# Kernel tuning notes

Measured on AMD Instinct MI355X. Metric: run time of the kernel, lower is better.

The kernel has to match this reference:

```python
import jax, jax.numpy as jnp
import numpy as np

IC = 196        # number of input channels / recurrence steps
B, N = 32, 8192 # batch, points per batch


def setup_inputs() -> dict:
    key = jax.random.key(0)
    ks = jax.random.split(key, 9)
    n = IC - 1  # 195 ReLU cells
    # stacked weights for the 195 distinct rnn cells: Linear(2,6)->ReLU->Linear(6,1)->ReLU
    W1 = jax.random.normal(ks[0], (n, 2, 6), dtype=jnp.float32) * (1.0 / np.sqrt(2.0))
    b1 = jax.random.normal(ks[1], (n, 6), dtype=jnp.float32) * 0.05
    W2 = jax.random.normal(ks[2], (n, 6, 1), dtype=jnp.float32) * (1.0 / np.sqrt(6.0))
    b2 = jax.random.normal(ks[3], (n, 1), dtype=jnp.float32) * 0.05
    # final sigmoid cell: Linear(2,6)->ReLU->Linear(6,1)->Sigmoid
    Wf1 = jax.random.normal(ks[4], (2, 6), dtype=jnp.float32) * (1.0 / np.sqrt(2.0))
    bf1 = jax.random.normal(ks[5], (6,), dtype=jnp.float32) * 0.05
    Wf2 = jax.random.normal(ks[6], (6, 1), dtype=jnp.float32) * (1.0 / np.sqrt(6.0))
    bf2 = jax.random.normal(ks[7], (1,), dtype=jnp.float32) * 0.05
    x = jax.random.normal(ks[8], (B, N, IC), dtype=jnp.float32)
    return {"x": x, "W1": W1, "b1": b1, "W2": W2, "b2": b2,
            "Wf1": Wf1, "bf1": bf1, "Wf2": Wf2, "bf2": bf2}


def reference(x, W1, b1, W2, b2, Wf1, bf1, Wf2, bf2):
    # x: [B, N, IC]. Recurrence: y0 = x[..., 0:1]; for i in 0..IC-2:
    #   y = relu_cell_i(concat(x[..., i:i+1], y));  final: sigmoid cell on x[..., IC-1].
    xs = jnp.moveaxis(x, -1, 0)          # [IC, B, N]
    y0 = xs[0][..., None]                # [B, N, 1]

    def step(y, inp):
        xi, w1, bb1, w2, bb2 = inp
        z = jnp.concatenate([xi[..., None], y], axis=-1)        # [B, N, 2]
        h = jax.nn.relu(jnp.einsum('bni,io->bno', z, w1) + bb1)  # [B, N, 6]
        y = jax.nn.relu(jnp.einsum('bnh,ho->bno', h, w2) + bb2)  # [B, N, 1]
        return y, None

    y, _ = jax.lax.scan(step, y0, (xs[:IC - 1], W1, b1, W2, b2))
    zf = jnp.concatenate([xs[IC - 1][..., None], y], axis=-1)    # [B, N, 2]
    hf = jax.nn.relu(jnp.einsum('bni,io->bno', zf, Wf1) + bf1)
    return jax.nn.sigmoid(jnp.einsum('bnh,ho->bno', hf, Wf2) + bf2)  # [B, N, 1]
```

## Files before the change

kernel.cpp:

```cpp
#include <hip/hip_runtime.h>
#include <math.h>

#define ICC 196
#define CH  16
#define NPH 12
#define RS  257
#define BLK 256

__device__ __forceinline__ float cell_step(float xi, float y, int i,
    const float* __restrict__ W1, const float* __restrict__ b1,
    const float* __restrict__ W2, const float* __restrict__ b2)
{
    const float* w1 = W1 + i * 12;
    const float* bb = b1 + i * 6;
    const float* w2 = W2 + i * 6;
    float h0 = fmaxf(fmaf(y, w1[6],  fmaf(xi, w1[0], bb[0])), 0.0f);
    float h1 = fmaxf(fmaf(y, w1[7],  fmaf(xi, w1[1], bb[1])), 0.0f);
    float h2 = fmaxf(fmaf(y, w1[8],  fmaf(xi, w1[2], bb[2])), 0.0f);
    float h3 = fmaxf(fmaf(y, w1[9],  fmaf(xi, w1[3], bb[3])), 0.0f);
    float h4 = fmaxf(fmaf(y, w1[10], fmaf(xi, w1[4], bb[4])), 0.0f);
    float h5 = fmaxf(fmaf(y, w1[11], fmaf(xi, w1[5], bb[5])), 0.0f);
    float a0 = fmaf(h0, w2[0], fmaf(h1, w2[1], b2[i]));
    float a1 = fmaf(h2, w2[2], h3 * w2[3]);
    float a2 = fmaf(h4, w2[4], h5 * w2[5]);
    return fmaxf(a0 + (a1 + a2), 0.0f);
}

__global__ __launch_bounds__(BLK, 4) void rnn_kernel(
    const float* __restrict__ x,
    const float* __restrict__ W1,
    const float* __restrict__ b1,
    const float* __restrict__ W2,
    const float* __restrict__ b2,
    const float* __restrict__ Wf1,
    const float* __restrict__ bf1,
    const float* __restrict__ Wf2,
    const float* __restrict__ bf2,
    float* __restrict__ out,
    int npoints)
{
    __shared__ float tile[CH * RS];

    const int tid = threadIdx.x;
    const int p0  = blockIdx.x * BLK;
    const int p   = p0 + tid;

    const int rl0 = tid >> 2;
    const int q4  = (tid & 3) * 4;

    float4 rA[4];

    const int pc_self = (p < npoints) ? p : (npoints - 1);
    const float4 tail = *reinterpret_cast<const float4*>(
        x + (size_t)pc_self * ICC + 192);

    #pragma unroll
    for (int k = 0; k < 4; ++k) {
        int rl = rl0 + 64 * k;
        int pc = p0 + rl; if (pc >= npoints) pc = npoints - 1;
        rA[k] = *reinterpret_cast<const float4*>(x + (size_t)pc * ICC + 0 * CH + q4);
    }
    #pragma unroll
    for (int k = 0; k < 4; ++k) {
        int rl = rl0 + 64 * k;
        tile[(q4 + 0) * RS + rl] = rA[k].x;
        tile[(q4 + 1) * RS + rl] = rA[k].y;
        tile[(q4 + 2) * RS + rl] = rA[k].z;
        tile[(q4 + 3) * RS + rl] = rA[k].w;
    }
    #pragma unroll
    for (int k = 0; k < 4; ++k) {
        int rl = rl0 + 64 * k;
        int pc = p0 + rl; if (pc >= npoints) pc = npoints - 1;
        rA[k] = *reinterpret_cast<const float4*>(x + (size_t)pc * ICC + 1 * CH + q4);
    }
    __syncthreads();

    float y = tile[0 * RS + tid];

    #pragma unroll 1
    for (int c = 0; c < NPH; ++c) {
        float xi[CH];
        #pragma unroll
        for (int j = 0; j < CH; ++j)
            xi[j] = tile[j * RS + tid];

        if (c < NPH - 1) {
            __syncthreads();
            #pragma unroll
            for (int k = 0; k < 4; ++k) {
                int rl = rl0 + 64 * k;
                tile[(q4 + 0) * RS + rl] = rA[k].x;
                tile[(q4 + 1) * RS + rl] = rA[k].y;
                tile[(q4 + 2) * RS + rl] = rA[k].z;
                tile[(q4 + 3) * RS + rl] = rA[k].w;
            }
            if (c < NPH - 2) {
                #pragma unroll
                for (int k = 0; k < 4; ++k) {
                    int rl = rl0 + 64 * k;
                    int pc = p0 + rl; if (pc >= npoints) pc = npoints - 1;
                    rA[k] = *reinterpret_cast<const float4*>(
                        x + (size_t)pc * ICC + (c + 2) * CH + q4);
                }
            }
            __syncthreads();
        }

        #pragma unroll
        for (int j = 0; j < CH; ++j)
            y = cell_step(xi[j], y, c * CH + j, W1, b1, W2, b2);
    }

    y = cell_step(tail.x, y, 192, W1, b1, W2, b2);
    y = cell_step(tail.y, y, 193, W1, b1, W2, b2);
    y = cell_step(tail.z, y, 194, W1, b1, W2, b2);

    const float xf = tail.w;
    float h0 = fmaxf(fmaf(y, Wf1[6],  fmaf(xf, Wf1[0], bf1[0])), 0.0f);
    float h1 = fmaxf(fmaf(y, Wf1[7],  fmaf(xf, Wf1[1], bf1[1])), 0.0f);
    float h2 = fmaxf(fmaf(y, Wf1[8],  fmaf(xf, Wf1[2], bf1[2])), 0.0f);
    float h3 = fmaxf(fmaf(y, Wf1[9],  fmaf(xf, Wf1[3], bf1[3])), 0.0f);
    float h4 = fmaxf(fmaf(y, Wf1[10], fmaf(xf, Wf1[4], bf1[4])), 0.0f);
    float h5 = fmaxf(fmaf(y, Wf1[11], fmaf(xf, Wf1[5], bf1[5])), 0.0f);
    float a0 = fmaf(h0, Wf2[0], fmaf(h1, Wf2[1], bf2[0]));
    float a1 = fmaf(h2, Wf2[2], h3 * Wf2[3]);
    float a2 = fmaf(h4, Wf2[4], h5 * Wf2[5]);
    float t  = a0 + (a1 + a2);

    if (p < npoints)
        out[p] = 1.0f / (1.0f + __expf(-t));
}

extern "C" void kernel_launch(void* const* d_in, const int* in_sizes, int n_in,
                              void* d_out, int out_size, void* d_ws, size_t ws_size,
                              hipStream_t stream) {
    const float* x   = (const float*)d_in[0];
    const float* W1  = (const float*)d_in[1];
    const float* b1  = (const float*)d_in[2];
    const float* W2  = (const float*)d_in[3];
    const float* b2  = (const float*)d_in[4];
    const float* Wf1 = (const float*)d_in[5];
    const float* bf1 = (const float*)d_in[6];
    const float* Wf2 = (const float*)d_in[7];
    const float* bf2 = (const float*)d_in[8];
    float* out = (float*)d_out;

    const int npoints = out_size;
    const int grid = (npoints + BLK - 1) / BLK;
    rnn_kernel<<<grid, BLK, 0, stream>>>(x, W1, b1, W2, b2,
                                         Wf1, bf1, Wf2, bf2, out, npoints);
}
```

Before: 104.6 us.

## Stage cell weights in LDS and double-buffer input chunks with explicit waitcnts

Copies all 195 cells' weights into shared memory once per block, padded to a 24-float stride, so each cell's weights come from vector LDS loads instead of scalar global loads. The input tile changes from a transposed column-major layout to a row-per-point layout read as float4. Two register buffers now alternate for the next chunk, and hand-placed s_waitcnt and s_barrier calls replace __syncthreads to overlap global loads with compute. This adds about 19KB of LDS per block, which may lower occupancy, and the inline-asm wait counts are fragile.

```diff
diff --git a/kernel.cpp b/kernel.cpp
--- a/kernel.cpp
+++ b/kernel.cpp
@@ -1,29 +1,40 @@
 #include <hip/hip_runtime.h>
 #include <math.h>
 
-#define ICC 196
-#define CH  16
-#define NPH 12
-#define RS  257
-#define BLK 256
+#define ICC   196
+#define CH    16
+#define NPH   12
+#define RS2   20
+#define BLK   256
+#define NCELL 195
+#define WSTR  24
 
-__device__ __forceinline__ float cell_step(float xi, float y, int i,
-    const float* __restrict__ W1, const float* __restrict__ b1,
-    const float* __restrict__ W2, const float* __restrict__ b2)
-{
-    const float* w1 = W1 + i * 12;
-    const float* bb = b1 + i * 6;
-    const float* w2 = W2 + i * 6;
-    float h0 = fmaxf(fmaf(y, w1[6],  fmaf(xi, w1[0], bb[0])), 0.0f);
-    float h1 = fmaxf(fmaf(y, w1[7],  fmaf(xi, w1[1], bb[1])), 0.0f);
-    float h2 = fmaxf(fmaf(y, w1[8],  fmaf(xi, w1[2], bb[2])), 0.0f);
-    float h3 = fmaxf(fmaf(y, w1[9],  fmaf(xi, w1[3], bb[3])), 0.0f);
-    float h4 = fmaxf(fmaf(y, w1[10], fmaf(xi, w1[4], bb[4])), 0.0f);
-    float h5 = fmaxf(fmaf(y, w1[11], fmaf(xi, w1[5], bb[5])), 0.0f);
-    float a0 = fmaf(h0, w2[0], fmaf(h1, w2[1], b2[i]));
-    float a1 = fmaf(h2, w2[2], h3 * w2[3]);
-    float a2 = fmaf(h4, w2[4], h5 * w2[5]);
-    return fmaxf(a0 + (a1 + a2), 0.0f);
+#define WAIT_VM(n)  asm volatile("s_waitcnt vmcnt(" #n ")" ::: "memory")
+#define WAIT_LGKM0  asm volatile("s_waitcnt lgkmcnt(0)" ::: "memory")
+#define SFENCE      __builtin_amdgcn_sched_barrier(0)
+#define SBAR        __builtin_amdgcn_s_barrier()
+
+struct WF { float4 q0,q1,q2,q3,q4,q5; float e0; };
+
+__device__ __forceinline__ WF loadWL(const float* wlds, const float* b2lds, int i) {
+    WF w;
+    const float4* b = reinterpret_cast<const float4*>(wlds + i * WSTR);
+    w.q0 = b[0]; w.q1 = b[1]; w.q2 = b[2]; w.q3 = b[3]; w.q4 = b[4]; w.q5 = b[5];
+    w.e0 = b2lds[i];
+    return w;
+}
+
+__device__ __forceinline__ float cellF(float xi, float y, const WF& w) {
+    float h0 = fmaxf(fmaf(y, w.q1.z, fmaf(xi, w.q0.x, w.q3.x)), 0.f);
+    float h1 = fmaxf(fmaf(y, w.q1.w, fmaf(xi, w.q0.y, w.q3.y)), 0.f);
+    float h2 = fmaxf(fmaf(y, w.q2.x, fmaf(xi, w.q0.z, w.q3.z)), 0.f);
+    float h3 = fmaxf(fmaf(y, w.q2.y, fmaf(xi, w.q0.w, w.q3.w)), 0.f);
+    float h4 = fmaxf(fmaf(y, w.q2.z, fmaf(xi, w.q1.x, w.q4.x)), 0.f);
+    float h5 = fmaxf(fmaf(y, w.q2.w, fmaf(xi, w.q1.y, w.q4.y)), 0.f);
+    float s0 = fmaf(h0, w.q4.z, fmaf(h1, w.q4.w, w.e0));
+    float s1 = fmaf(h2, w.q5.x, h3 * w.q5.y);
+    float s2 = fmaf(h4, w.q5.z, h5 * w.q5.w);
+    return fmaxf(s0 + (s1 + s2), 0.f);
 }
 
 __global__ __launch_bounds__(BLK, 4) void rnn_kernel(
@@ -39,82 +50,116 @@
     float* __restrict__ out,
     int npoints)
 {
-    __shared__ float tile[CH * RS];
+    __shared__ float wlds[NCELL * WSTR];
+    __shared__ float b2lds[NCELL];
+    __shared__ float tile[BLK * RS2];
 
     const int tid = threadIdx.x;
     const int p0  = blockIdx.x * BLK;
     const int p   = p0 + tid;
 
+    for (int i = tid; i < NCELL * 3; i += BLK) {
+        int cell = i / 3, part = i - cell * 3;
+        float4 v = reinterpret_cast<const float4*>(W1)[i];
+        *reinterpret_cast<float4*>(&wlds[cell * WSTR + part * 4]) = v;
+    }
+    for (int i = tid; i < NCELL * 3; i += BLK) {
+        int cell = i / 3, part = i - cell * 3;
+        float2 v = reinterpret_cast<const float2*>(b1)[i];
+        *reinterpret_cast<float2*>(&wlds[cell * WSTR + 12 + part * 2]) = v;
+    }
+    for (int i = tid; i < NCELL * 3; i += BLK) {
+        int cell = i / 3, part = i - cell * 3;
+        float2 v = reinterpret_cast<const float2*>(W2)[i];
+        *reinterpret_cast<float2*>(&wlds[cell * WSTR + 18 + part * 2]) = v;
+    }
+    for (int i = tid; i < NCELL; i += BLK) b2lds[i] = b2[i];
+
     const int rl0 = tid >> 2;
-    const int q4  = (tid & 3) * 4;
+    const int cq  = (tid & 3) * 4;
 
-    float4 rA[4];
-
-    const int pc_self = (p < npoints) ? p : (npoints - 1);
-    const float4 tail = *reinterpret_cast<const float4*>(
-        x + (size_t)pc_self * ICC + 192);
+    float4 rA[4], rB[4];
 
     #pragma unroll
     for (int k = 0; k < 4; ++k) {
         int rl = rl0 + 64 * k;
         int pc = p0 + rl; if (pc >= npoints) pc = npoints - 1;
-        rA[k] = *reinterpret_cast<const float4*>(x + (size_t)pc * ICC + 0 * CH + q4);
-    }
-    #pragma unroll
-    for (int k = 0; k < 4; ++k) {
-        int rl = rl0 + 64 * k;
-        tile[(q4 + 0) * RS + rl] = rA[k].x;
-        tile[(q4 + 1) * RS + rl] = rA[k].y;
-        tile[(q4 + 2) * RS + rl] = rA[k].z;
-        tile[(q4 + 3) * RS + rl] = rA[k].w;
+        rA[k] = *reinterpret_cast<const float4*>(x + (size_t)pc * ICC + 0 * CH + cq);
     }
     #pragma unroll
     for (int k = 0; k < 4; ++k) {
         int rl = rl0 + 64 * k;
         int pc = p0 + rl; if (pc >= npoints) pc = npoints - 1;
-        rA[k] = *reinterpret_cast<const float4*>(x + (size_t)pc * ICC + 1 * CH + q4);
+        rB[k] = *reinterpret_cast<const float4*>(x + (size_t)pc * ICC + 1 * CH + cq);
     }
-    __syncthreads();
+    const int pc_self = (p < npoints) ? p : (npoints - 1);
+    const float4 tail = *reinterpret_cast<const float4*>(
+        x + (size_t)pc_self * ICC + 192);
+    SFENCE;
 
-    float y = tile[0 * RS + tid];
+    WAIT_VM(5); SFENCE;
+    #pragma unroll
+    for (int k = 0; k < 4; ++k)
+        *reinterpret_cast<float4*>(&tile[(rl0 + 64 * k) * RS2 + cq]) = rA[k];
+    WAIT_LGKM0; SFENCE;
+    SBAR;
+
+    float y = tile[tid * RS2];
+
+    auto phase = [&](int c, float4 (&cur)[4], float4 (&nxt)[4]) {
+        float4 xi4[4];
+        #pragma unroll
+        for (int k = 0; k < 4; ++k)
+            xi4[k] = *reinterpret_cast<const float4*>(&tile[tid * RS2 + 4 * k]);
+        WAIT_LGKM0; SFENCE;
+        SBAR;
+
+        int cc = (c + 2 < NPH) ? (c + 2) : (NPH - 1);
+        #pragma unroll
+        for (int k = 0; k < 4; ++k) {
+            int rl = rl0 + 64 * k;
+            int pc = p0 + rl; if (pc >= npoints) pc = npoints - 1;
+            nxt[k] = *reinterpret_cast<const float4*>(
+                x + (size_t)pc * ICC + cc * CH + cq);
+        }
+        SFENCE;
+        WAIT_VM(4); SFENCE;
+        #pragma unroll
+        for (int k = 0; k < 4; ++k)
+            *reinterpret_cast<float4*>(&tile[(rl0 + 64 * k) * RS2 + cq]) = cur[k];
+        WAIT_LGKM0; SFENCE;
+        SBAR;
+
+        const float xi[CH] = { xi4[0].x, xi4[0].y, xi4[0].z, xi4[0].w,
+                               xi4[1].x, xi4[1].y, xi4[1].z, xi4[1].w,
+                               xi4[2].x, xi4[2].y, xi4[2].z, xi4[2].w,
+                               xi4[3].x, xi4[3].y, xi4[3].z, xi4[3].w };
+
+        WF wA = loadWL(wlds, b2lds, c * CH + 0);
+        WF wB = loadWL(wlds, b2lds, c * CH + 1);
+        #pragma unroll
+        for (int j = 0; j < CH; j += 2) {
+            y = cellF(xi[j], y, wA);
+            if (j + 2 < CH) wA = loadWL(wlds, b2lds, c * CH + j + 2);
+            y = cellF(xi[j + 1], y, wB);
+            if (j + 3 < CH) wB = loadWL(wlds, b2lds, c * CH + j + 3);
+        }
+    };
 
     #pragma unroll 1
-    for (int c = 0; c < NPH; ++c) {
-        float xi[CH];
-        #pragma unroll
-        for (int j = 0; j < CH; ++j)
-            xi[j] = tile[j * RS + tid];
-
-        if (c < NPH - 1) {
-            __syncthreads();
-            #pragma unroll
-            for (int k = 0; k < 4; ++k) {
-                int rl = rl0 + 64 * k;
-                tile[(q4 + 0) * RS + rl] = rA[k].x;
-                tile[(q4 + 1) * RS + rl] = rA[k].y;
-                tile[(q4 + 2) * RS + rl] = rA[k].z;
-                tile[(q4 + 3) * RS + rl] = rA[k].w;
-            }
-            if (c < NPH - 2) {
-                #pragma unroll
-                for (int k = 0; k < 4; ++k) {
-                    int rl = rl0 + 64 * k;
-                    int pc = p0 + rl; if (pc >= npoints) pc = npoints - 1;
-                    rA[k] = *reinterpret_cast<const float4*>(
-                        x + (size_t)pc * ICC + (c + 2) * CH + q4);
-                }
-            }
-            __syncthreads();
-        }
-
-        #pragma unroll
-        for (int j = 0; j < CH; ++j)
-            y = cell_step(xi[j], y, c * CH + j, W1, b1, W2, b2);
+    for (int c2 = 0; c2 < NPH; c2 += 2) {
+        phase(c2,     rB, rA);
+        phase(c2 + 1, rA, rB);
     }
 
-    y = cell_step(tail.x, y, 192, W1, b1, W2, b2);
-    y = cell_step(tail.y, y, 193, W1, b1, W2, b2);
-    y = cell_step(tail.z, y, 194, W1, b1, W2, b2);
+    {
+        WF w0 = loadWL(wlds, b2lds, 192);
+        WF w1c = loadWL(wlds, b2lds, 193);
+        WF w2c = loadWL(wlds, b2lds, 194);
+        y = cellF(tail.x, y, w0);
+        y = cellF(tail.y, y, w1c);
+        y = cellF(tail.z, y, w2c);
+    }
 
     const float xf = tail.w;
     float h0 = fmaxf(fmaf(y, Wf1[6],  fmaf(xf, Wf1[0], bf1[0])), 0.0f);
@@ -123,10 +168,10 @@
     float h3 = fmaxf(fmaf(y, Wf1[9],  fmaf(xf, Wf1[3], bf1[3])), 0.0f);
     float h4 = fmaxf(fmaf(y, Wf1[10], fmaf(xf, Wf1[4], bf1[4])), 0.0f);
     float h5 = fmaxf(fmaf(y, Wf1[11], fmaf(xf, Wf1[5], bf1[5])), 0.0f);
-    float a0 = fmaf(h0, Wf2[0], fmaf(h1, Wf2[1], bf2[0]));
-    float a1 = fmaf(h2, Wf2[2], h3 * Wf2[3]);
-    float a2 = fmaf(h4, Wf2[4], h5 * Wf2[5]);
-    float t  = a0 + (a1 + a2);
+    float s0 = fmaf(h0, Wf2[0], fmaf(h1, Wf2[1], bf2[0]));
+    float s1 = fmaf(h2, Wf2[2], h3 * Wf2[3]);
+    float s2 = fmaf(h4, Wf2[4], h5 * Wf2[5]);
+    float t  = s0 + (s1 + s2);
 
     if (p < npoints)
         out[p] = 1.0f / (1.0f + __expf(-t));
```

Result: slower. 161.2 us (+54.2%).
